# Optimization experiments

Hardware: AMD Instinct MI355X
Metric: run time of the kernel (lower is better)

Reference implementation:

```python
import jax, jax.numpy as jnp
import numpy as np
from jax.ops import segment_sum

GRID = 32        # cells per axis; offset grid is (GRID+1)^3
T = 48           # number of accepted MC topologies
N_PTS = 131072

# 12 cube edges: base (lower) corner offset and axis the edge runs along.
# e0..3: x/y edges of z=0 face, e4..7: same at z=1, e8..11: vertical z edges.
EDGE_BASE = np.array([[0,0,0],[1,0,0],[0,1,0],[0,0,0],
                      [0,0,1],[1,0,1],[0,1,1],[0,0,1],
                      [0,0,0],[1,0,0],[1,1,0],[0,1,0]], dtype=np.int32)
EDGE_AXIS = np.array([0,1,0,1, 0,1,0,1, 2,2,2,2], dtype=np.int32)
EDGE_DIR  = np.eye(3, dtype=np.float32)[EDGE_AXIS]          # [12,3] unit dirs


def _dot(u, v):
    return jnp.sum(u * v, axis=-1)


def _safe_div(n, d, eps=1e-12):
    return n / jnp.where(jnp.abs(d) > eps, d, eps)


def _point_tri_dist_sq(p, a, b, c):
    """Squared distance from p to triangle (a,b,c); Ericson closest-point
    algorithm with full vertex/edge/interior region clamping, vectorized.
    p broadcasts against a/b/c over leading dims; last dim is xyz."""
    ab = b - a; ac = c - a; ap = p - a
    d1 = _dot(ab, ap); d2 = _dot(ac, ap)
    bp = p - b; d3 = _dot(ab, bp); d4 = _dot(ac, bp)
    cp = p - c; d5 = _dot(ab, cp); d6 = _dot(ac, cp)
    vc = d1 * d4 - d3 * d2
    vb = d5 * d2 - d1 * d6
    va = d3 * d6 - d5 * d4
    v_ab = _safe_div(d1, d1 - d3)
    w_ac = _safe_div(d2, d2 - d6)
    w_bc = _safe_div(d4 - d3, (d4 - d3) + (d5 - d6))
    inv = _safe_div(jnp.ones_like(va), va + vb + vc)
    v_in = vb * inv; w_in = vc * inv
    q = a + ab * v_in[..., None] + ac * w_in[..., None]                      # interior
    q = jnp.where(((va <= 0) & ((d4 - d3) >= 0) & ((d5 - d6) >= 0))[..., None],
                  b + (c - b) * w_bc[..., None], q)                          # edge BC
    q = jnp.where(((vb <= 0) & (d2 >= 0) & (d6 <= 0))[..., None],
                  a + ac * w_ac[..., None], q)                               # edge AC
    q = jnp.where(((d6 >= 0) & (d5 <= d6))[..., None], c, q)                 # vertex C
    q = jnp.where(((vc <= 0) & (d1 >= 0) & (d3 <= 0))[..., None],
                  a + ab * v_ab[..., None], q)                               # edge AB
    q = jnp.where(((d3 >= 0) & (d4 <= d3))[..., None], b, q)                 # vertex B
    q = jnp.where(((d1 <= 0) & (d2 <= 0))[..., None], a, q)                  # vertex A
    diff = p - q
    return _dot(diff, diff)


def setup_inputs() -> dict:
    key = jax.random.key(0)
    k1, k2, k3 = jax.random.split(key, 3)
    offset = jax.random.uniform(k1, (3, GRID + 1, GRID + 1, GRID + 1), dtype=jnp.float32)
    points = jax.random.uniform(k2, (N_PTS, 3), dtype=jnp.float32) * GRID
    tri_table = jax.random.randint(k3, (T, 3, 3), 0, 12, dtype=jnp.int32)
    return {"offset": offset, "points": points, "tri_table": tri_table}


def reference(offset, points, tri_table):
    edge_base_i = jnp.asarray(EDGE_BASE)                 # [12,3] int
    edge_base_f = jnp.asarray(EDGE_BASE, dtype=offset.dtype)
    edge_dir = jnp.asarray(EDGE_DIR, dtype=offset.dtype)
    edge_axis = jnp.asarray(EDGE_AXIS)

    cell = jnp.clip(jnp.floor(points).astype(jnp.int32), 0, GRID - 1)   # [N,3]
    local = points - cell.astype(points.dtype)                          # [N,3] in [0,1)^3

    # grid index of each edge's base corner -> edge offset parameter t in [0,1]
    gidx = cell[:, None, :] + edge_base_i[None, :, :]                   # [N,12,3]
    t = offset[edge_axis[None, :], gidx[..., 0], gidx[..., 1], gidx[..., 2]]  # [N,12]
    verts = edge_base_f[None] + edge_dir[None] * t[..., None]           # [N,12,3] local coords

    tri = verts[:, tri_table]                                           # [N,T,3tri,3vert,3]
    a = tri[:, :, :, 0, :]; b = tri[:, :, :, 1, :]; c = tri[:, :, :, 2, :]
    p = local[:, None, None, :]                                         # [N,1,1,3]
    d2 = _point_tri_dist_sq(p, a, b, c)                                 # [N,T,3]
    d_min = jnp.min(d2, axis=-1)                                        # [N,T]

    cell_id = (cell[:, 0] * GRID + cell[:, 1]) * GRID + cell[:, 2]      # [N]
    distances_full = segment_sum(d_min, cell_id, num_segments=GRID ** 3)  # [GRID^3, T]
    return distances_full
```

## Files before the change

### kernel.cpp

```cpp
#include <hip/hip_runtime.h>

#define GRID 32
#define NT 48
#define BLK 256
#define SPLIT 16
#define PPB (BLK / SPLIT)

#define EDGE_PACK ( (0ULL<<0) | (9ULL<<5) | (2ULL<<10) | (8ULL<<15) | \
                    (4ULL<<20) | (13ULL<<25) | (6ULL<<30) | (12ULL<<35) | \
                    (16ULL<<40) | (17ULL<<45) | (19ULL<<50) | (18ULL<<55) )

__device__ float tri_dist_sq(float Apx, float Apy, float Apz,
                             float Bpx, float Bpy, float Bpz,
                             float Cpx, float Cpy, float Cpz) {
    float abx = Apx - Bpx, aby = Apy - Bpy, abz = Apz - Bpz;
    float acx = Apx - Cpx, acy = Apy - Cpy, acz = Apz - Cpz;
    float d1 = abx * Apx + aby * Apy + abz * Apz;
    float d2 = acx * Apx + acy * Apy + acz * Apz;
    float d3 = abx * Bpx + aby * Bpy + abz * Bpz;
    float d4 = acx * Bpx + acy * Bpy + acz * Bpz;
    float d5 = abx * Cpx + aby * Cpy + abz * Cpz;
    float d6 = acx * Cpx + acy * Cpy + acz * Cpz;
    float vc = d1 * d4 - d3 * d2;
    float vb = d5 * d2 - d1 * d6;
    float va = d3 * d6 - d5 * d4;
    float d43 = d4 - d3;
    float d56 = d5 - d6;

    bool c_bc = (va <= 0.0f) & (d43 >= 0.0f) & (d56 >= 0.0f);
    bool c_ac = (vb <= 0.0f) & (d2 >= 0.0f) & (d6 <= 0.0f);
    bool c_c  = (d6 >= 0.0f) & (d5 <= d6);
    bool c_ab = (vc <= 0.0f) & (d1 >= 0.0f) & (d3 <= 0.0f);
    bool c_b  = (d3 >= 0.0f) & (d4 <= d3);
    bool c_a  = (d1 <= 0.0f) & (d2 <= 0.0f);

    float den = va + vb + vc;
    den = c_bc ? (d43 + d56) : den;
    den = c_ac ? (d2 - d6)   : den;
    den = c_c  ? 1.0f        : den;
    den = c_ab ? (d1 - d3)   : den;
    den = (c_b | c_a) ? 1.0f : den;
    den = (fabsf(den) > 1e-12f) ? den : 1e-12f;
    float r = __builtin_amdgcn_rcpf(den);

    float nw = vc;
    nw = c_bc ? d43  : nw;
    nw = c_ac ? d2   : nw;
    nw = c_c  ? 1.0f : nw;
    nw = (c_ab | c_b | c_a) ? 0.0f : nw;

    float nv = vb;
    nv = c_bc ? (den - d43) : nv;
    nv = (c_ac | c_c) ? 0.0f : nv;
    nv = c_ab ? d1   : nv;
    nv = c_b  ? 1.0f : nv;
    nv = c_a  ? 0.0f : nv;

    float v = nv * r;
    float w = nw * r;
    float dx = Apx - abx * v - acx * w;
    float dy = Apy - aby * v - acy * w;
    float dz = Apz - abz * v - acz * w;
    return dx * dx + dy * dy + dz * dz;
}

__global__ __launch_bounds__(BLK) void ptd_kernel(
    const float* __restrict__ offset,
    const float* __restrict__ points,
    const int*   __restrict__ tri_table,
    float*       __restrict__ out,
    int n)
{
    __shared__ float4 v_s[PPB * 13];
    __shared__ int t_tab[NT * 3];

    const int tid = threadIdx.x;
    const int g   = blockIdx.x * BLK + tid;
    const int pt  = g >> 4;
    const int grp = tid & 15;
    const int pl  = tid >> 4;
    const bool active = (pt < n);

    if (tid < NT * 3) {
        int i0 = tri_table[tid * 3 + 0];
        int i1 = tri_table[tid * 3 + 1];
        int i2 = tri_table[tid * 3 + 2];
        t_tab[tid] = i0 | (i1 << 8) | (i2 << 16);
    }

    int cx = 0, cy = 0, cz = 0;
    if (active) {
        float px = points[pt * 3 + 0];
        float py = points[pt * 3 + 1];
        float pz = points[pt * 3 + 2];
        cx = min(max((int)floorf(px), 0), GRID - 1);
        cy = min(max((int)floorf(py), 0), GRID - 1);
        cz = min(max((int)floorf(pz), 0), GRID - 1);
        if (grp < 12) {
            float lx = px - (float)cx;
            float ly = py - (float)cy;
            float lz = pz - (float)cz;
            unsigned nib = (unsigned)(EDGE_PACK >> (5 * grp)) & 31u;
            int gx = cx + (int)(nib & 1u);
            int gy = cy + (int)((nib >> 1) & 1u);
            int gz = cz + (int)((nib >> 2) & 1u);
            int ax = (int)(nib >> 3);
            float t = offset[((ax * 33 + gx) * 33 + gy) * 33 + gz];
            float vx = (ax == 0) ? t : (float)(nib & 1u);
            float vy = (ax == 1) ? t : (float)((nib >> 1) & 1u);
            float vz = (ax == 2) ? t : (float)((nib >> 2) & 1u);
            v_s[pl * 13 + grp] = make_float4(lx - vx, ly - vy, lz - vz, 0.0f);
        }
    }
    __syncthreads();

    if (!active) return;

    const float4* vrow = &v_s[pl * 13];
    float* outp = out + ((((cx * GRID) + cy) * GRID + cz) * NT);

#pragma unroll
    for (int r = 0; r < 3; r++) {
        const int t = grp * 3 + r;
        float dmin;
#pragma unroll
        for (int k = 0; k < 3; k++) {
            int packed = t_tab[t * 3 + k];
            float4 A = vrow[packed & 255];
            float4 B = vrow[(packed >> 8) & 255];
            float4 C = vrow[(packed >> 16) & 255];
            float d = tri_dist_sq(A.x, A.y, A.z, B.x, B.y, B.z, C.x, C.y, C.z);
            dmin = (k == 0) ? d : fminf(dmin, d);
        }
        atomicAdd(&outp[t], dmin);
    }
}

extern "C" void kernel_launch(void* const* d_in, const int* in_sizes, int n_in,
                              void* d_out, int out_size, void* d_ws, size_t ws_size,
                              hipStream_t stream) {
    const float* offset    = (const float*)d_in[0];
    const float* points    = (const float*)d_in[1];
    const int*   tri_table = (const int*)d_in[2];
    float* out = (float*)d_out;
    int n = in_sizes[1] / 3;

    hipMemsetAsync(d_out, 0, (size_t)out_size * sizeof(float), stream);

    long total = (long)n * SPLIT;
    int blocks = (int)((total + BLK - 1) / BLK);
    ptd_kernel<<<blocks, BLK, 0, stream>>>(offset, points, tri_table, out, n);
}
```

Before: 127.2 us.

## Remap threads so each wave covers 64 points with wave-uniform topology rows

Result: slower. 404.3 us (+217.8%).

```diff
diff --git a/kernel.cpp b/kernel.cpp
--- a/kernel.cpp
+++ b/kernel.cpp
@@ -3,30 +3,31 @@
 #define GRID 32
 #define NT 48
 #define BLK 256
-#define SPLIT 16
-#define PPB (BLK / SPLIT)
+#define PPB 64
+#define RPW 12
 
 #define EDGE_PACK ( (0ULL<<0) | (9ULL<<5) | (2ULL<<10) | (8ULL<<15) | \
                     (4ULL<<20) | (13ULL<<25) | (6ULL<<30) | (12ULL<<35) | \
                     (16ULL<<40) | (17ULL<<45) | (19ULL<<50) | (18ULL<<55) )
 
-__device__ float tri_dist_sq(float Apx, float Apy, float Apz,
-                             float Bpx, float Bpy, float Bpz,
-                             float Cpx, float Cpy, float Cpz) {
-    float abx = Apx - Bpx, aby = Apy - Bpy, abz = Apz - Bpz;
-    float acx = Apx - Cpx, acy = Apy - Cpy, acz = Apz - Cpz;
-    float d1 = abx * Apx + aby * Apy + abz * Apz;
-    float d2 = acx * Apx + acy * Apy + acz * Apz;
-    float d3 = abx * Bpx + aby * Bpy + abz * Bpz;
-    float d4 = acx * Bpx + acy * Bpy + acz * Bpz;
-    float d5 = abx * Cpx + aby * Cpy + abz * Cpz;
-    float d6 = acx * Cpx + acy * Cpy + acz * Cpz;
-    float vc = d1 * d4 - d3 * d2;
-    float vb = d5 * d2 - d1 * d6;
-    float va = d3 * d6 - d5 * d4;
-    float d43 = d4 - d3;
-    float d56 = d5 - d6;
-
+__device__ __forceinline__ float tri_dist_sq(float4 A, float4 B, float4 C) {
+    float abx = A.x - B.x, aby = A.y - B.y, abz = A.z - B.z;
+    float acx = A.x - C.x, acy = A.y - C.y, acz = A.z - C.z;
+    float d1, d2, d3, d4, d5, d6, va, vb, vc, d43, d56;
+    {
+#pragma clang fp contract(off)
+        d1 = (abx * A.x + aby * A.y) + abz * A.z;
+        d2 = (acx * A.x + acy * A.y) + acz * A.z;
+        d3 = (abx * B.x + aby * B.y) + abz * B.z;
+        d4 = (acx * B.x + acy * B.y) + acz * B.z;
+        d5 = (abx * C.x + aby * C.y) + abz * C.z;
+        d6 = (acx * C.x + acy * C.y) + acz * C.z;
+        vc = d1 * d4 - d3 * d2;
+        vb = d5 * d2 - d1 * d6;
+        va = d3 * d6 - d5 * d4;
+        d43 = d4 - d3;
+        d56 = d5 - d6;
+    }
     bool c_bc = (va <= 0.0f) & (d43 >= 0.0f) & (d56 >= 0.0f);
     bool c_ac = (vb <= 0.0f) & (d2 >= 0.0f) & (d6 <= 0.0f);
     bool c_c  = (d6 >= 0.0f) & (d5 <= d6);
@@ -58,9 +59,9 @@
 
     float v = nv * r;
     float w = nw * r;
-    float dx = Apx - abx * v - acx * w;
-    float dy = Apy - aby * v - acy * w;
-    float dz = Apz - abz * v - acz * w;
+    float dx = A.x - abx * v - acx * w;
+    float dy = A.y - aby * v - acy * w;
+    float dz = A.z - abz * v - acz * w;
     return dx * dx + dy * dy + dz * dz;
 }
 
@@ -74,11 +75,10 @@
     __shared__ float4 v_s[PPB * 13];
     __shared__ int t_tab[NT * 3];
 
-    const int tid = threadIdx.x;
-    const int g   = blockIdx.x * BLK + tid;
-    const int pt  = g >> 4;
-    const int grp = tid & 15;
-    const int pl  = tid >> 4;
+    const int tid  = threadIdx.x;
+    const int lane = tid & 63;
+    const int wv   = tid >> 6;
+    const int pt   = blockIdx.x * PPB + lane;
     const bool active = (pt < n);
 
     if (tid < NT * 3) {
@@ -96,11 +96,13 @@
         cx = min(max((int)floorf(px), 0), GRID - 1);
         cy = min(max((int)floorf(py), 0), GRID - 1);
         cz = min(max((int)floorf(pz), 0), GRID - 1);
-        if (grp < 12) {
-            float lx = px - (float)cx;
-            float ly = py - (float)cy;
-            float lz = pz - (float)cz;
-            unsigned nib = (unsigned)(EDGE_PACK >> (5 * grp)) & 31u;
+        float lx = px - (float)cx;
+        float ly = py - (float)cy;
+        float lz = pz - (float)cz;
+#pragma unroll
+        for (int j = 0; j < 3; j++) {
+            int e = wv * 3 + j;
+            unsigned nib = (unsigned)(EDGE_PACK >> (5 * e)) & 31u;
             int gx = cx + (int)(nib & 1u);
             int gy = cy + (int)((nib >> 1) & 1u);
             int gz = cz + (int)((nib >> 2) & 1u);
@@ -109,30 +111,30 @@
             float vx = (ax == 0) ? t : (float)(nib & 1u);
             float vy = (ax == 1) ? t : (float)((nib >> 1) & 1u);
             float vz = (ax == 2) ? t : (float)((nib >> 2) & 1u);
-            v_s[pl * 13 + grp] = make_float4(lx - vx, ly - vy, lz - vz, 0.0f);
+            v_s[lane * 13 + e] = make_float4(lx - vx, ly - vy, lz - vz, 0.0f);
         }
     }
     __syncthreads();
 
     if (!active) return;
 
-    const float4* vrow = &v_s[pl * 13];
+    const float4* vrow = &v_s[lane * 13];
     float* outp = out + ((((cx * GRID) + cy) * GRID + cz) * NT);
 
-#pragma unroll
-    for (int r = 0; r < 3; r++) {
-        const int t = grp * 3 + r;
-        float dmin;
-#pragma unroll
-        for (int k = 0; k < 3; k++) {
-            int packed = t_tab[t * 3 + k];
-            float4 A = vrow[packed & 255];
-            float4 B = vrow[(packed >> 8) & 255];
-            float4 C = vrow[(packed >> 16) & 255];
-            float d = tri_dist_sq(A.x, A.y, A.z, B.x, B.y, B.z, C.x, C.y, C.z);
-            dmin = (k == 0) ? d : fminf(dmin, d);
-        }
-        atomicAdd(&outp[t], dmin);
+    for (int rr = 0; rr < RPW; rr++) {
+        const int row = wv * RPW + rr;
+        int p0 = __builtin_amdgcn_readfirstlane(t_tab[row * 3 + 0]);
+        int p1 = __builtin_amdgcn_readfirstlane(t_tab[row * 3 + 1]);
+        int p2 = __builtin_amdgcn_readfirstlane(t_tab[row * 3 + 2]);
+        float4 A0 = vrow[p0 & 255], B0 = vrow[(p0 >> 8) & 255], C0 = vrow[(p0 >> 16) & 255];
+        float4 A1 = vrow[p1 & 255], B1 = vrow[(p1 >> 8) & 255], C1 = vrow[(p1 >> 16) & 255];
+        float d0 = tri_dist_sq(A0, B0, C0);
+        float4 A2 = vrow[p2 & 255], B2 = vrow[(p2 >> 8) & 255], C2 = vrow[(p2 >> 16) & 255];
+        float d1 = tri_dist_sq(A1, B1, C1);
+        float dmin = fminf(d0, d1);
+        float d2 = tri_dist_sq(A2, B2, C2);
+        dmin = fminf(dmin, d2);
+        atomicAdd(&outp[row], dmin);
     }
 }
 
@@ -147,7 +149,6 @@
 
     hipMemsetAsync(d_out, 0, (size_t)out_size * sizeof(float), stream);
 
-    long total = (long)n * SPLIT;
-    int blocks = (int)((total + BLK - 1) / BLK);
+    int blocks = (n + PPB - 1) / PPB;
     ptd_kernel<<<blocks, BLK, 0, stream>>>(offset, points, tri_table, out, n);
 }
```

## Replace global float atomics with cell-sorted scratch and per-cell segmented reduction

Applied to the files above, without the earlier changes.

New measurement: 163.4 us. 1.28x slower.

```diff
diff --git a/kernel.cpp b/kernel.cpp
--- a/kernel.cpp
+++ b/kernel.cpp
@@ -1,6 +1,7 @@
 #include <hip/hip_runtime.h>
 
 #define GRID 32
+#define NCELL (GRID * GRID * GRID)
 #define NT 48
 #define BLK 256
 #define SPLIT 16
@@ -10,23 +11,28 @@
                     (4ULL<<20) | (13ULL<<25) | (6ULL<<30) | (12ULL<<35) | \
                     (16ULL<<40) | (17ULL<<45) | (19ULL<<50) | (18ULL<<55) )
 
-__device__ float tri_dist_sq(float Apx, float Apy, float Apz,
-                             float Bpx, float Bpy, float Bpz,
-                             float Cpx, float Cpy, float Cpz) {
-    float abx = Apx - Bpx, aby = Apy - Bpy, abz = Apz - Bpz;
-    float acx = Apx - Cpx, acy = Apy - Cpy, acz = Apz - Cpz;
-    float d1 = abx * Apx + aby * Apy + abz * Apz;
-    float d2 = acx * Apx + acy * Apy + acz * Apz;
-    float d3 = abx * Bpx + aby * Bpy + abz * Bpz;
-    float d4 = acx * Bpx + acy * Bpy + acz * Bpz;
-    float d5 = abx * Cpx + aby * Cpy + abz * Cpz;
-    float d6 = acx * Cpx + acy * Cpy + acz * Cpz;
-    float vc = d1 * d4 - d3 * d2;
-    float vb = d5 * d2 - d1 * d6;
-    float va = d3 * d6 - d5 * d4;
-    float d43 = d4 - d3;
-    float d56 = d5 - d6;
-
+__device__ __forceinline__ int cell_of(float p) {
+    return min(max((int)floorf(p), 0), GRID - 1);
+}
+
+__device__ __forceinline__ float tri_dist_sq(float4 A, float4 B, float4 C) {
+    float abx = A.x - B.x, aby = A.y - B.y, abz = A.z - B.z;
+    float acx = A.x - C.x, acy = A.y - C.y, acz = A.z - C.z;
+    float d1, d2, d3, d4, d5, d6, va, vb, vc, d43, d56;
+    {
+#pragma clang fp contract(off)
+        d1 = (abx * A.x + aby * A.y) + abz * A.z;
+        d2 = (acx * A.x + acy * A.y) + acz * A.z;
+        d3 = (abx * B.x + aby * B.y) + abz * B.z;
+        d4 = (acx * B.x + acy * B.y) + acz * B.z;
+        d5 = (abx * C.x + aby * C.y) + abz * C.z;
+        d6 = (acx * C.x + acy * C.y) + acz * C.z;
+        vc = d1 * d4 - d3 * d2;
+        vb = d5 * d2 - d1 * d6;
+        va = d3 * d6 - d5 * d4;
+        d43 = d4 - d3;
+        d56 = d5 - d6;
+    }
     bool c_bc = (va <= 0.0f) & (d43 >= 0.0f) & (d56 >= 0.0f);
     bool c_ac = (vb <= 0.0f) & (d2 >= 0.0f) & (d6 <= 0.0f);
     bool c_c  = (d6 >= 0.0f) & (d5 <= d6);
@@ -58,17 +64,64 @@
 
     float v = nv * r;
     float w = nw * r;
-    float dx = Apx - abx * v - acx * w;
-    float dy = Apy - aby * v - acy * w;
-    float dz = Apz - abz * v - acz * w;
+    float dx = A.x - abx * v - acx * w;
+    float dy = A.y - aby * v - acy * w;
+    float dz = A.z - abz * v - acz * w;
     return dx * dx + dy * dy + dz * dz;
 }
 
-__global__ __launch_bounds__(BLK) void ptd_kernel(
+
+__global__ void hist_kernel(const float* __restrict__ pts, int* __restrict__ cnt, int n) {
+    int i = blockIdx.x * blockDim.x + threadIdx.x;
+    if (i >= n) return;
+    int cx = cell_of(pts[3 * i + 0]);
+    int cy = cell_of(pts[3 * i + 1]);
+    int cz = cell_of(pts[3 * i + 2]);
+    atomicAdd(&cnt[(cx * GRID + cy) * GRID + cz], 1);
+}
+
+__global__ __launch_bounds__(1024) void scan_kernel(
+    const int* __restrict__ cnt, int* __restrict__ start, int* __restrict__ cursor) {
+    __shared__ int part[1024];
+    const int tid = threadIdx.x;
+    const int base = tid * 32;
+    int s = 0;
+    for (int j = 0; j < 32; j++) s += cnt[base + j];
+    part[tid] = s;
+    __syncthreads();
+    for (int off = 1; off < 1024; off <<= 1) {
+        int add = (tid >= off) ? part[tid - off] : 0;
+        __syncthreads();
+        part[tid] += add;
+        __syncthreads();
+    }
+    int run = (tid == 0) ? 0 : part[tid - 1];
+    for (int j = 0; j < 32; j++) {
+        int c = cnt[base + j];
+        start[base + j]  = run;
+        cursor[base + j] = run;
+        run += c;
+    }
+    if (tid == 1023) start[NCELL] = run;
+}
+
+__global__ void scatter_kernel(const float* __restrict__ pts, int* __restrict__ cursor,
+                               int* __restrict__ sorted, int n) {
+    int i = blockIdx.x * blockDim.x + threadIdx.x;
+    if (i >= n) return;
+    int cx = cell_of(pts[3 * i + 0]);
+    int cy = cell_of(pts[3 * i + 1]);
+    int cz = cell_of(pts[3 * i + 2]);
+    int pos = atomicAdd(&cursor[(cx * GRID + cy) * GRID + cz], 1);
+    sorted[pos] = i;
+}
+
+__global__ __launch_bounds__(BLK) void compute_kernel(
     const float* __restrict__ offset,
     const float* __restrict__ points,
     const int*   __restrict__ tri_table,
-    float*       __restrict__ out,
+    const int*   __restrict__ sorted,
+    float*       __restrict__ scratch,
     int n)
 {
     __shared__ float4 v_s[PPB * 13];
@@ -76,10 +129,10 @@
 
     const int tid = threadIdx.x;
     const int g   = blockIdx.x * BLK + tid;
-    const int pt  = g >> 4;
+    const int sp  = g >> 4;
     const int grp = tid & 15;
     const int pl  = tid >> 4;
-    const bool active = (pt < n);
+    const bool active = (sp < n);
 
     if (tid < NT * 3) {
         int i0 = tri_table[tid * 3 + 0];
@@ -88,14 +141,12 @@
         t_tab[tid] = i0 | (i1 << 8) | (i2 << 16);
     }
 
-    int cx = 0, cy = 0, cz = 0;
     if (active) {
+        int pt = sorted[sp];
         float px = points[pt * 3 + 0];
         float py = points[pt * 3 + 1];
         float pz = points[pt * 3 + 2];
-        cx = min(max((int)floorf(px), 0), GRID - 1);
-        cy = min(max((int)floorf(py), 0), GRID - 1);
-        cz = min(max((int)floorf(pz), 0), GRID - 1);
+        int cx = cell_of(px), cy = cell_of(py), cz = cell_of(pz);
         if (grp < 12) {
             float lx = px - (float)cx;
             float ly = py - (float)cy;
@@ -117,7 +168,7 @@
     if (!active) return;
 
     const float4* vrow = &v_s[pl * 13];
-    float* outp = out + ((((cx * GRID) + cy) * GRID + cz) * NT);
+    float* outp = scratch + (size_t)sp * NT;
 
 #pragma unroll
     for (int r = 0; r < 3; r++) {
@@ -129,7 +180,80 @@
             float4 A = vrow[packed & 255];
             float4 B = vrow[(packed >> 8) & 255];
             float4 C = vrow[(packed >> 16) & 255];
-            float d = tri_dist_sq(A.x, A.y, A.z, B.x, B.y, B.z, C.x, C.y, C.z);
+            float d = tri_dist_sq(A, B, C);
+            dmin = (k == 0) ? d : fminf(dmin, d);
+        }
+        outp[t] = dmin;
+    }
+}
+
+__global__ void reduce_kernel(const int* __restrict__ start,
+                              const float* __restrict__ scratch,
+                              float* __restrict__ out) {
+    int g = blockIdx.x * blockDim.x + threadIdx.x;
+    if (g >= NCELL * NT) return;
+    int cell = g / NT;
+    int t    = g - cell * NT;
+    int s0 = start[cell], s1 = start[cell + 1];
+    float acc = 0.0f;
+    for (int i = s0; i < s1; i++) acc += scratch[(size_t)i * NT + t];
+    out[g] = acc;
+}
+
+
+__global__ __launch_bounds__(BLK) void atomic_kernel(
+    const float* __restrict__ offset, const float* __restrict__ points,
+    const int* __restrict__ tri_table, float* __restrict__ out, int n)
+{
+    __shared__ float4 v_s[PPB * 13];
+    __shared__ int t_tab[NT * 3];
+    const int tid = threadIdx.x;
+    const int g   = blockIdx.x * BLK + tid;
+    const int pt  = g >> 4;
+    const int grp = tid & 15;
+    const int pl  = tid >> 4;
+    const bool active = (pt < n);
+    if (tid < NT * 3) {
+        int i0 = tri_table[tid * 3 + 0];
+        int i1 = tri_table[tid * 3 + 1];
+        int i2 = tri_table[tid * 3 + 2];
+        t_tab[tid] = i0 | (i1 << 8) | (i2 << 16);
+    }
+    int cx = 0, cy = 0, cz = 0;
+    if (active) {
+        float px = points[pt * 3 + 0];
+        float py = points[pt * 3 + 1];
+        float pz = points[pt * 3 + 2];
+        cx = cell_of(px); cy = cell_of(py); cz = cell_of(pz);
+        if (grp < 12) {
+            float lx = px - (float)cx, ly = py - (float)cy, lz = pz - (float)cz;
+            unsigned nib = (unsigned)(EDGE_PACK >> (5 * grp)) & 31u;
+            int gx = cx + (int)(nib & 1u);
+            int gy = cy + (int)((nib >> 1) & 1u);
+            int gz = cz + (int)((nib >> 2) & 1u);
+            int ax = (int)(nib >> 3);
+            float t = offset[((ax * 33 + gx) * 33 + gy) * 33 + gz];
+            float vx = (ax == 0) ? t : (float)(nib & 1u);
+            float vy = (ax == 1) ? t : (float)((nib >> 1) & 1u);
+            float vz = (ax == 2) ? t : (float)((nib >> 2) & 1u);
+            v_s[pl * 13 + grp] = make_float4(lx - vx, ly - vy, lz - vz, 0.0f);
+        }
+    }
+    __syncthreads();
+    if (!active) return;
+    const float4* vrow = &v_s[pl * 13];
+    float* outp = out + ((((cx * GRID) + cy) * GRID + cz) * NT);
+#pragma unroll
+    for (int r = 0; r < 3; r++) {
+        const int t = grp * 3 + r;
+        float dmin;
+#pragma unroll
+        for (int k = 0; k < 3; k++) {
+            int packed = t_tab[t * 3 + k];
+            float4 A = vrow[packed & 255];
+            float4 B = vrow[(packed >> 8) & 255];
+            float4 C = vrow[(packed >> 16) & 255];
+            float d = tri_dist_sq(A, B, C);
             dmin = (k == 0) ? d : fminf(dmin, d);
         }
         atomicAdd(&outp[t], dmin);
@@ -145,9 +269,27 @@
     float* out = (float*)d_out;
     int n = in_sizes[1] / 3;
 
-    hipMemsetAsync(d_out, 0, (size_t)out_size * sizeof(float), stream);
-
-    long total = (long)n * SPLIT;
-    int blocks = (int)((total + BLK - 1) / BLK);
-    ptd_kernel<<<blocks, BLK, 0, stream>>>(offset, points, tri_table, out, n);
-}
+    size_t need = ((size_t)NCELL * 2 + (NCELL + 1) + n + (size_t)n * NT) * 4;
+    if (ws_size >= need) {
+        int* cnt    = (int*)d_ws;
+        int* cursor = cnt + NCELL;
+        int* start  = cursor + NCELL;
+        int* sorted = start + (NCELL + 1);
+        float* scratch = (float*)(sorted + n);
+
+        hipMemsetAsync(cnt, 0, NCELL * sizeof(int), stream);
+        int pblk = (n + 255) / 256;
+        hist_kernel<<<pblk, 256, 0, stream>>>(points, cnt, n);
+        scan_kernel<<<1, 1024, 0, stream>>>(cnt, start, cursor);
+        scatter_kernel<<<pblk, 256, 0, stream>>>(points, cursor, sorted, n);
+        long total = (long)n * SPLIT;
+        compute_kernel<<<(int)((total + BLK - 1) / BLK), BLK, 0, stream>>>(
+            offset, points, tri_table, sorted, scratch, n);
+        reduce_kernel<<<(NCELL * NT + 255) / 256, 256, 0, stream>>>(start, scratch, out);
+    } else {
+        hipMemsetAsync(d_out, 0, (size_t)out_size * sizeof(float), stream);
+        long total = (long)n * SPLIT;
+        atomic_kernel<<<(int)((total + BLK - 1) / BLK), BLK, 0, stream>>>(
+            offset, points, tri_table, out, n);
+    }
+}
```
